# Optimization experiments

Hardware: AMD Instinct MI355X
Metric: run time of the kernel (lower is better)

The kernel has to match this reference:

```python
import jax, jax.numpy as jnp
import numpy as np


def setup_inputs() -> dict:
    key = jax.random.key(0)
    ks = jax.random.split(key, 8)
    B, M, C, H, W = 2, 16, 256, 64, 64
    T = 1024  # transformer_dim
    return {
        "transformer_output": jax.random.normal(ks[0], (B, T), dtype=jnp.float32),
        "residual_maps": jax.random.normal(ks[1], (B, M, C, H, W), dtype=jnp.float32),
        "Wq": jax.random.normal(ks[2], (C, T), dtype=jnp.float32) * 0.02,
        "bq": jnp.zeros((C,), dtype=jnp.float32),
        "Wk": jax.random.normal(ks[3], (C, C), dtype=jnp.float32) * 0.02,
        "bk": jnp.zeros((C,), dtype=jnp.float32),
        "Wv": jax.random.normal(ks[4], (C, C), dtype=jnp.float32) * 0.02,
        "bv": jnp.zeros((C,), dtype=jnp.float32),
    }


def reference(transformer_output, residual_maps, Wq, bq, Wk, bk, Wv, bv):
    # residual_maps: [B, M, C, H, W]; single query per batch element.
    B, M, C, H, W = residual_maps.shape
    scale = C ** (-0.5)
    # Linear query projection: [B, C]
    q = transformer_output @ Wq.T + bq
    # 1x1 conv == per-pixel channel matmul: [B, M, C, H, W]
    keys = jnp.einsum("oc,bmchw->bmohw", Wk, residual_maps) + bk[None, None, :, None, None]
    values = jnp.einsum("oc,bmchw->bmohw", Wv, residual_maps) + bv[None, None, :, None, None]
    # Single-query dot-product scores per (map, pixel): [B, M, H, W]
    scores = jnp.einsum("bc,bmchw->bmhw", q, keys) * scale
    # Temporal softmax over num_maps at each spatial position
    probs = jax.nn.softmax(scores, axis=1)
    # Softmax-weighted sum of value maps: [B, C, H, W]
    out = jnp.einsum("bmhw,bmchw->bchw", probs, values)
    return out
```

## Files before the change

kernel.cpp:

```cpp
#include <hip/hip_runtime.h>

#define SCALE 0.0625f

typedef __attribute__((ext_vector_type(4))) float f32x4;
typedef __attribute__((ext_vector_type(8))) short s16x8;

__device__ __forceinline__ unsigned short f2bf(float x) {
    unsigned u = __float_as_uint(x);
    u = u + 0x7FFF + ((u >> 16) & 1);
    return (unsigned short)(u >> 16);
}

__global__ __launch_bounds__(256) void prep1_kernel(
    const float* __restrict__ TO,
    const float* __restrict__ Wq,
    const float* __restrict__ bq,
    const float* __restrict__ Wv,
    float* __restrict__ qbuf,
    unsigned short* __restrict__ WvB)
{
    const int blk = blockIdx.x;
    const int t   = threadIdx.x;
    if (blk < 16) {
        const int b    = blk >> 3;
        const int rblk = blk & 7;
        const int wv = t >> 6, l = t & 63;
        const float4* Wq4 = (const float4*)Wq;
        const float4* TO4 = (const float4*)TO;
        for (int rr = 0; rr < 8; ++rr) {
            const int c = rblk * 32 + wv * 8 + rr;
            float acc = 0.f;
#pragma unroll
            for (int i = 0; i < 4; ++i) {
                float4 wq = Wq4[c * 256 + i * 64 + l];
                float4 tv = TO4[b * 256 + i * 64 + l];
                acc = fmaf(wq.x, tv.x, acc);
                acc = fmaf(wq.y, tv.y, acc);
                acc = fmaf(wq.z, tv.z, acc);
                acc = fmaf(wq.w, tv.w, acc);
            }
#pragma unroll
            for (int mask = 1; mask < 64; mask <<= 1)
                acc += __shfl_xor(acc, mask, 64);
            if (l == 0) qbuf[b * 256 + c] = acc + bq[c];
        }
    } else {
        const int idx = blk - 16;
#pragma unroll
        for (int i = 0; i < 4; ++i) {
            const int e = idx * 4096 + i * 1024 + t * 4;
            const float4 f = ((const float4*)Wv)[e >> 2];
            ushort4 o;
            o.x = f2bf(f.x); o.y = f2bf(f.y);
            o.z = f2bf(f.z); o.w = f2bf(f.w);
            *(ushort4*)(WvB + e) = o;
        }
    }
}

__global__ __launch_bounds__(256) void prep2_kernel(
    const float* __restrict__ qbuf,
    const float* __restrict__ Wk,
    float* __restrict__ qks)
{
    const int blk = blockIdx.x;
    const int t   = threadIdx.x;
    const int b = blk >> 3, j = blk & 7;
    const int col = t & 31, chunk = t >> 5;
    const int cp = j * 32 + col;
    float partial = 0.f;
#pragma unroll 8
    for (int cc = 0; cc < 32; ++cc) {
        const int c = chunk * 32 + cc;
        partial = fmaf(qbuf[b * 256 + c], Wk[c * 256 + cp], partial);
    }
    __shared__ float r2[8][32];
    r2[chunk][col] = partial;
    __syncthreads();
    if (t < 32) {
        float s = 0.f;
#pragma unroll
        for (int k = 0; k < 8; ++k) s += r2[k][t];
        qks[b * 256 + j * 32 + t] = SCALE * s;
    }
}

__global__ __launch_bounds__(64, 1) void main_kernel(
    const float* __restrict__ X,
    const float* __restrict__ qks,
    const unsigned short* __restrict__ WvB,
    const float* __restrict__ bv,
    float* __restrict__ out)
{
    const int t   = threadIdx.x;
    const int blk = blockIdx.x;
    const int pb  = ((blk & 7) << 6) | (blk >> 3);
    const int b   = pb >> 8;
    const int hw0 = (pb & 255) << 4;
    const int p4  = t & 3;
    const int cg  = t >> 2;

    __shared__ float slab[256 * 20];

    float qk[16];
#pragma unroll
    for (int k = 0; k < 16; ++k) qk[k] = qks[b * 256 + cg + 16 * k];

    const float4* X4 = (const float4*)X;
    const int base0 = (b * 16) * 262144 + (hw0 >> 2) + p4;

    float4 v[2][16];
    float4 wx[16];
#pragma unroll
    for (int k = 0; k < 16; ++k) wx[k] = make_float4(0.f, 0.f, 0.f, 0.f);
    float lsum[4] = {0.f, 0.f, 0.f, 0.f};

#pragma unroll
    for (int k = 0; k < 16; ++k)
        v[0][k] = X4[base0 + (cg + 16 * k) * 1024];

#pragma unroll
    for (int m = 0; m < 16; ++m) {
        const int buf = m & 1, nxt = buf ^ 1;
        if (m < 15) {
#pragma unroll
            for (int k = 0; k < 16; ++k)
                v[nxt][k] = X4[base0 + (m + 1) * 262144 + (cg + 16 * k) * 1024];
        }
        float sx = 0.f, sy = 0.f, sz = 0.f, sw = 0.f;
#pragma unroll
        for (int k = 0; k < 16; ++k) {
            sx = fmaf(qk[k], v[buf][k].x, sx);
            sy = fmaf(qk[k], v[buf][k].y, sy);
            sz = fmaf(qk[k], v[buf][k].z, sz);
            sw = fmaf(qk[k], v[buf][k].w, sw);
        }
#pragma unroll
        for (int mask = 4; mask < 64; mask <<= 1) {
            sx += __shfl_xor(sx, mask, 64);
            sy += __shfl_xor(sy, mask, 64);
            sz += __shfl_xor(sz, mask, 64);
            sw += __shfl_xor(sw, mask, 64);
        }
        const float w0 = __expf(sx), w1 = __expf(sy);
        const float w2 = __expf(sz), w3 = __expf(sw);
        lsum[0] += w0; lsum[1] += w1; lsum[2] += w2; lsum[3] += w3;
#pragma unroll
        for (int k = 0; k < 16; ++k) {
            wx[k].x = fmaf(w0, v[buf][k].x, wx[k].x);
            wx[k].y = fmaf(w1, v[buf][k].y, wx[k].y);
            wx[k].z = fmaf(w2, v[buf][k].z, wx[k].z);
            wx[k].w = fmaf(w3, v[buf][k].w, wx[k].w);
        }
    }

    const float i0 = 1.0f / lsum[0], i1 = 1.0f / lsum[1];
    const float i2 = 1.0f / lsum[2], i3 = 1.0f / lsum[3];
#pragma unroll
    for (int k = 0; k < 16; ++k) {
        *(float4*)&slab[(cg + 16 * k) * 20 + 4 * p4] =
            make_float4(wx[k].x * i0, wx[k].y * i1, wx[k].z * i2, wx[k].w * i3);
    }
    __syncthreads();

    const int px   = t & 15;
    const int quad = t >> 4;

    f32x4 acc[16];
#pragma unroll
    for (int tt = 0; tt < 16; ++tt) {
#pragma unroll
        for (int r = 0; r < 4; ++r)
            acc[tt][r] = bv[16 * tt + quad * 4 + r];
    }

#pragma unroll
    for (int ks = 0; ks < 8; ++ks) {
        s16x8 bfr;
#pragma unroll
        for (int j = 0; j < 8; ++j)
            bfr[j] = (short)f2bf(slab[(ks * 32 + quad * 8 + j) * 20 + px]);
#pragma unroll
        for (int tt = 0; tt < 16; ++tt) {
            const s16x8 afr =
                *(const s16x8*)(WvB + (16 * tt + px) * 256 + ks * 32 + quad * 8);
            acc[tt] = __builtin_amdgcn_mfma_f32_16x16x32_bf16(afr, bfr, acc[tt],
                                                              0, 0, 0);
        }
    }

    const int obase = b * 256 * 4096 + hw0;
#pragma unroll
    for (int tt = 0; tt < 16; ++tt) {
#pragma unroll
        for (int r = 0; r < 4; ++r) {
            const int co = 16 * tt + quad * 4 + r;
            out[obase + co * 4096 + px] = acc[tt][r];
        }
    }
}

extern "C" void kernel_launch(void* const* d_in, const int* in_sizes, int n_in,
                              void* d_out, int out_size, void* d_ws, size_t ws_size,
                              hipStream_t stream) {
    const float* TO = (const float*)d_in[0];
    const float* X  = (const float*)d_in[1];
    const float* Wq = (const float*)d_in[2];
    const float* bq = (const float*)d_in[3];
    const float* Wk = (const float*)d_in[4];
    const float* Wv = (const float*)d_in[6];
    const float* bv = (const float*)d_in[7];
    float* out = (float*)d_out;
    float* ws  = (float*)d_ws;

    float*          qbuf = ws;
    float*          qks  = ws + 512;
    unsigned short* WvB  = (unsigned short*)(ws + 1024);

    hipLaunchKernelGGL(prep1_kernel, dim3(32), dim3(256), 0, stream,
                       TO, Wq, bq, Wv, qbuf, WvB);
    hipLaunchKernelGGL(prep2_kernel, dim3(16), dim3(256), 0, stream,
                       qbuf, Wk, qks);
    hipLaunchKernelGGL(main_kernel, dim3(512), dim3(64), 0, stream,
                       X, qks, WvB, bv, out);
}
```

Measured before the change: 242.0 us.

## Split score computation into separate kernel and widen main kernel to 256 threads

Computes per-pixel attention scores in a standalone kernel, then a second kernel reads the scores, applies softmax, and accumulates the weighted sum and value projection with four waves per block instead of one. The old design used a single 64-thread wave per block that held 16 float4 per buffer in registers, which limited occupancy. The cost is reading the residual maps twice (about 128 MB each pass) plus an extra launch, in exchange for more parallelism and lower register pressure.

```diff
diff --git a/kernel.cpp b/kernel.cpp
--- a/kernel.cpp
+++ b/kernel.cpp
@@ -85,9 +85,30 @@
     }
 }
 
-__global__ __launch_bounds__(64, 1) void main_kernel(
+__global__ __launch_bounds__(256) void scores_kernel(
     const float* __restrict__ X,
     const float* __restrict__ qks,
+    float* __restrict__ scores)
+{
+    const int blk = blockIdx.x;
+    const int bm  = blk >> 4;
+    const int px  = ((blk & 15) << 8) + threadIdx.x;
+    const float* __restrict__ Xr = X + bm * 1048576 + px;
+    const float* __restrict__ qr = qks + (bm >> 4) * 256;
+    float s0 = 0.f, s1 = 0.f, s2 = 0.f, s3 = 0.f;
+#pragma unroll 4
+    for (int c = 0; c < 256; c += 4) {
+        s0 = fmaf(qr[c + 0], Xr[(c + 0) * 4096], s0);
+        s1 = fmaf(qr[c + 1], Xr[(c + 1) * 4096], s1);
+        s2 = fmaf(qr[c + 2], Xr[(c + 2) * 4096], s2);
+        s3 = fmaf(qr[c + 3], Xr[(c + 3) * 4096], s3);
+    }
+    scores[bm * 4096 + px] = (s0 + s1) + (s2 + s3);
+}
+
+__global__ __launch_bounds__(256) void wxconv_kernel(
+    const float* __restrict__ X,
+    const float* __restrict__ scores,
     const unsigned short* __restrict__ WvB,
     const float* __restrict__ bv,
     float* __restrict__ out)
@@ -97,81 +118,78 @@
     const int pb  = ((blk & 7) << 6) | (blk >> 3);
     const int b   = pb >> 8;
     const int hw0 = (pb & 255) << 4;
-    const int p4  = t & 3;
-    const int cg  = t >> 2;
-
+
+    __shared__ float pl[16][16];
+    __shared__ float invl[16];
     __shared__ float slab[256 * 20];
 
-    float qk[16];
-#pragma unroll
-    for (int k = 0; k < 16; ++k) qk[k] = qks[b * 256 + cg + 16 * k];
-
+    {
+        const int px_s = t & 15, m_s = t >> 4;
+        const float e = __expf(scores[(b * 16 + m_s) * 4096 + hw0 + px_s]);
+        pl[m_s][px_s] = e;
+        __syncthreads();
+        if (t < 16) {
+            float s = 0.f;
+#pragma unroll
+            for (int m = 0; m < 16; ++m) s += pl[m][t];
+            invl[t] = 1.0f / s;
+        }
+        __syncthreads();
+        pl[m_s][px_s] *= invl[px_s];
+        __syncthreads();
+    }
+
+    const int p4 = t & 3;
+    const int cg = t >> 2;
     const float4* X4 = (const float4*)X;
     const int base0 = (b * 16) * 262144 + (hw0 >> 2) + p4;
 
-    float4 v[2][16];
-    float4 wx[16];
-#pragma unroll
-    for (int k = 0; k < 16; ++k) wx[k] = make_float4(0.f, 0.f, 0.f, 0.f);
-    float lsum[4] = {0.f, 0.f, 0.f, 0.f};
-
-#pragma unroll
-    for (int k = 0; k < 16; ++k)
-        v[0][k] = X4[base0 + (cg + 16 * k) * 1024];
+    float4 v[2][4];
+    float4 wx[4];
+#pragma unroll
+    for (int k = 0; k < 4; ++k) wx[k] = make_float4(0.f, 0.f, 0.f, 0.f);
+
+#pragma unroll
+    for (int k = 0; k < 4; ++k)
+        v[0][k] = X4[base0 + (cg + 64 * k) * 1024];
+    float4 pm[2];
+    pm[0] = *(const float4*)&pl[0][4 * p4];
 
 #pragma unroll
     for (int m = 0; m < 16; ++m) {
         const int buf = m & 1, nxt = buf ^ 1;
         if (m < 15) {
 #pragma unroll
-            for (int k = 0; k < 16; ++k)
-                v[nxt][k] = X4[base0 + (m + 1) * 262144 + (cg + 16 * k) * 1024];
-        }
-        float sx = 0.f, sy = 0.f, sz = 0.f, sw = 0.f;
-#pragma unroll
-        for (int k = 0; k < 16; ++k) {
-            sx = fmaf(qk[k], v[buf][k].x, sx);
-            sy = fmaf(qk[k], v[buf][k].y, sy);
-            sz = fmaf(qk[k], v[buf][k].z, sz);
-            sw = fmaf(qk[k], v[buf][k].w, sw);
-        }
-#pragma unroll
-        for (int mask = 4; mask < 64; mask <<= 1) {
-            sx += __shfl_xor(sx, mask, 64);
-            sy += __shfl_xor(sy, mask, 64);
-            sz += __shfl_xor(sz, mask, 64);
-            sw += __shfl_xor(sw, mask, 64);
-        }
-        const float w0 = __expf(sx), w1 = __expf(sy);
-        const float w2 = __expf(sz), w3 = __expf(sw);
-        lsum[0] += w0; lsum[1] += w1; lsum[2] += w2; lsum[3] += w3;
-#pragma unroll
-        for (int k = 0; k < 16; ++k) {
-            wx[k].x = fmaf(w0, v[buf][k].x, wx[k].x);
-            wx[k].y = fmaf(w1, v[buf][k].y, wx[k].y);
-            wx[k].z = fmaf(w2, v[buf][k].z, wx[k].z);
-            wx[k].w = fmaf(w3, v[buf][k].w, wx[k].w);
-        }
-    }
-
-    const float i0 = 1.0f / lsum[0], i1 = 1.0f / lsum[1];
-    const float i2 = 1.0f / lsum[2], i3 = 1.0f / lsum[3];
-#pragma unroll
-    for (int k = 0; k < 16; ++k) {
-        *(float4*)&slab[(cg + 16 * k) * 20 + 4 * p4] =
-            make_float4(wx[k].x * i0, wx[k].y * i1, wx[k].z * i2, wx[k].w * i3);
-    }
+            for (int k = 0; k < 4; ++k)
+                v[nxt][k] = X4[base0 + (m + 1) * 262144 + (cg + 64 * k) * 1024];
+            pm[nxt] = *(const float4*)&pl[m + 1][4 * p4];
+        }
+#pragma unroll
+        for (int k = 0; k < 4; ++k) {
+            wx[k].x = fmaf(pm[buf].x, v[buf][k].x, wx[k].x);
+            wx[k].y = fmaf(pm[buf].y, v[buf][k].y, wx[k].y);
+            wx[k].z = fmaf(pm[buf].z, v[buf][k].z, wx[k].z);
+            wx[k].w = fmaf(pm[buf].w, v[buf][k].w, wx[k].w);
+        }
+    }
+
+#pragma unroll
+    for (int k = 0; k < 4; ++k)
+        *(float4*)&slab[(cg + 64 * k) * 20 + 4 * p4] = wx[k];
     __syncthreads();
 
-    const int px   = t & 15;
-    const int quad = t >> 4;
-
-    f32x4 acc[16];
-#pragma unroll
-    for (int tt = 0; tt < 16; ++tt) {
+    const int w    = t >> 6;
+    const int lane = t & 63;
+    const int px   = lane & 15;
+    const int quad = lane >> 4;
+
+    f32x4 acc[4];
+#pragma unroll
+    for (int i = 0; i < 4; ++i) {
+        const int tt = 4 * w + i;
 #pragma unroll
         for (int r = 0; r < 4; ++r)
-            acc[tt][r] = bv[16 * tt + quad * 4 + r];
+            acc[i][r] = bv[16 * tt + quad * 4 + r];
     }
 
 #pragma unroll
@@ -181,21 +199,23 @@
         for (int j = 0; j < 8; ++j)
             bfr[j] = (short)f2bf(slab[(ks * 32 + quad * 8 + j) * 20 + px]);
 #pragma unroll
-        for (int tt = 0; tt < 16; ++tt) {
+        for (int i = 0; i < 4; ++i) {
+            const int tt = 4 * w + i;
             const s16x8 afr =
                 *(const s16x8*)(WvB + (16 * tt + px) * 256 + ks * 32 + quad * 8);
-            acc[tt] = __builtin_amdgcn_mfma_f32_16x16x32_bf16(afr, bfr, acc[tt],
-                                                              0, 0, 0);
-        }
-    }
-
-    const int obase = b * 256 * 4096 + hw0;
-#pragma unroll
-    for (int tt = 0; tt < 16; ++tt) {
+            acc[i] = __builtin_amdgcn_mfma_f32_16x16x32_bf16(afr, bfr, acc[i],
+                                                             0, 0, 0);
+        }
+    }
+
+    const int obase = b * 1048576 + hw0;
+#pragma unroll
+    for (int i = 0; i < 4; ++i) {
+        const int tt = 4 * w + i;
 #pragma unroll
         for (int r = 0; r < 4; ++r) {
             const int co = 16 * tt + quad * 4 + r;
-            out[obase + co * 4096 + px] = acc[tt][r];
+            out[obase + co * 4096 + px] = acc[i][r];
         }
     }
 }
@@ -213,14 +233,17 @@
     float* out = (float*)d_out;
     float* ws  = (float*)d_ws;
 
-    float*          qbuf = ws;
-    float*          qks  = ws + 512;
-    unsigned short* WvB  = (unsigned short*)(ws + 1024);
+    float*          qbuf   = ws;
+    float*          qks    = ws + 512;
+    unsigned short* WvB    = (unsigned short*)(ws + 1024);
+    float*          scores = ws + 1024 + 32768;
 
     hipLaunchKernelGGL(prep1_kernel, dim3(32), dim3(256), 0, stream,
                        TO, Wq, bq, Wv, qbuf, WvB);
     hipLaunchKernelGGL(prep2_kernel, dim3(16), dim3(256), 0, stream,
                        qbuf, Wk, qks);
-    hipLaunchKernelGGL(main_kernel, dim3(512), dim3(64), 0, stream,
-                       X, qks, WvB, bv, out);
-}
+    hipLaunchKernelGGL(scores_kernel, dim3(512), dim3(256), 0, stream,
+                       X, qks, scores);
+    hipLaunchKernelGGL(wxconv_kernel, dim3(512), dim3(256), 0, stream,
+                       X, scores, WvB, bv, out);
+}
```

Result: slower. 251.0 us (+3.7%).
